# Optimization experiments

Measured on AMD Instinct MI355X. Metric: run time of the kernel, lower is better.

The kernel has to match this reference:

```python
import jax, jax.numpy as jnp
import numpy as np
import math

WINDOW = 2048
EMBED = 1024
BATCH = 8


def setup_inputs() -> dict:
    key = jax.random.key(0)
    ks = jax.random.split(key, 7)
    s = 1.0 / math.sqrt(EMBED)
    return {
        "embeddings": jax.random.normal(ks[0], (BATCH, WINDOW, EMBED), dtype=jnp.float32),
        "Wq": jax.random.uniform(ks[1], (EMBED, EMBED), jnp.float32, -s, s),
        "bq": jax.random.uniform(ks[2], (EMBED,), jnp.float32, -s, s),
        "Wk": jax.random.uniform(ks[3], (EMBED, EMBED), jnp.float32, -s, s),
        "bk": jax.random.uniform(ks[4], (EMBED,), jnp.float32, -s, s),
        "Wv": jax.random.uniform(ks[5], (EMBED, EMBED), jnp.float32, -s, s),
        "bv": jax.random.uniform(ks[6], (EMBED,), jnp.float32, -s, s),
    }


def reference(embeddings, Wq, bq, Wk, bk, Wv, bv):
    # Linear layers: x @ W.T + b (torch nn.Linear convention)
    Q = jnp.einsum('bse,fe->bsf', embeddings, Wq) + bq
    K = jnp.einsum('bse,fe->bsf', embeddings, Wk) + bk
    V = jnp.einsum('bse,fe->bsf', embeddings, Wv) + bv
    scale = 1.0 / math.sqrt(EMBED)
    # [B, S, S] score matrix: A[b, i, j] = Q_i . K_j / sqrt(d)
    A = jnp.einsum('bie,bje->bij', Q, K) * scale
    # causal additive mask: -inf where j > i (strictly upper triangular)
    mask = jnp.triu(jnp.full((WINDOW, WINDOW), -jnp.inf, dtype=A.dtype), k=1)
    A = A + mask
    # NOTE: faithful to original nn.Softmax(dim=1): normalize over QUERY axis
    P = jax.nn.softmax(A, axis=1)
    return jnp.einsum('bij,bje->bie', P, V)
```

## Files before the change

kernel.cpp:

```cpp
#include <hip/hip_runtime.h>
#include <stdint.h>

#define WINDOW 2048
#define EMBED  1024
#define BATCH  8
#define MTOT   (BATCH*WINDOW)

typedef unsigned short u16;
typedef __bf16 bf16x8 __attribute__((ext_vector_type(8)));
typedef float  f32x4  __attribute__((ext_vector_type(4)));

#define BM 256
#define BN 256
#define BK 64
#define HALF 8192
#define KSCALE 0.04508422717564447f

#define WAITVM4 asm volatile("s_waitcnt vmcnt(4)" ::: "memory")
#define WAITVM0 asm volatile("s_waitcnt vmcnt(0)" ::: "memory")

__device__ __forceinline__ u16 f2bf(float f) {
  union { float f; unsigned u; } a; a.f = f;
  unsigned r = a.u + 0x7FFF + ((a.u >> 16) & 1);
  return (u16)(r >> 16);
}
__device__ __forceinline__ float bf2f(u16 u) {
  union { unsigned u; float f; } a; a.u = ((unsigned)u) << 16;
  return a.f;
}

__device__ __forceinline__ void gload16(const u16* g, u16* l) {
  __builtin_amdgcn_global_load_lds(
      (const __attribute__((address_space(1))) unsigned int*)g,
      (__attribute__((address_space(3))) unsigned int*)l, 16, 0, 0);
}

__device__ __forceinline__ void stage_half(const u16* g, int ld, int kkc,
                                           u16* lb, int tid) {
  #pragma unroll
  for (int h = 0; h < 2; ++h) {
    int f = h * 512 + tid;
    int r = f >> 2, c = f & 3;
    gload16(g + (size_t)r * ld + kkc * 32 + ((c ^ ((r >> 1) & 3)) << 3),
            lb + f * 8);
  }
}

__device__ __forceinline__ void gemm256(
    const u16* __restrict__ A, int lda,
    const u16* __restrict__ B, int ldb,
    int nt, u16* lds, f32x4 acc[8][4])
{
  const int tid  = threadIdx.x;
  const int lane = tid & 63;
  const int wid  = tid >> 6;
  const int wm   = (wid >> 2) * 128;
  const int wn   = (wid & 3) * 64;
  const int lrow = lane & 15;
  const int hi   = lane >> 4;
  u16* LDA = lds;
  u16* LDB = lds + 4 * HALF;

  stage_half(A, lda, 0, LDA + 0 * HALF, tid);
  stage_half(B, ldb, 0, LDB + 0 * HALF, tid);
  stage_half(A, lda, 1, LDA + 1 * HALF, tid);
  stage_half(B, ldb, 1, LDB + 1 * HALF, tid);
  WAITVM4;
  __builtin_amdgcn_s_barrier();

  for (int t = 0; t < nt; ++t) {
    const int buf = (t & 1) * 2;
    const int nb  = ((t + 1) & 1) * 2;
    u16* LA0 = LDA + buf * HALF;
    u16* LA1 = LA0 + HALF;
    u16* LB0 = LDB + buf * HALF;
    u16* LB1 = LB0 + HALF;
    const bool s  = (t + 1) < nt;
    const u16* An = A + (size_t)(t + 1) * BK;
    const u16* Bn = B + (size_t)(t + 1) * BK;

    bf16x8 av[4], bv[4];

    #pragma unroll
    for (int mi = 0; mi < 4; ++mi) {
      int r = wm + mi * 16 + lrow;
      av[mi] = *(const bf16x8*)(LA0 + r * 32 + ((hi ^ ((r >> 1) & 3)) << 3));
    }
    #pragma unroll
    for (int ni = 0; ni < 4; ++ni) {
      int r = wn + ni * 16 + lrow;
      bv[ni] = *(const bf16x8*)(LB0 + r * 32 + ((hi ^ ((r >> 1) & 3)) << 3));
    }
    if (s) stage_half(An, lda, 0, LDA + nb * HALF, tid);
    __builtin_amdgcn_s_barrier();
    __builtin_amdgcn_s_setprio(1);
    #pragma unroll
    for (int mi = 0; mi < 4; ++mi)
      #pragma unroll
      for (int ni = 0; ni < 4; ++ni)
        acc[mi][ni] = __builtin_amdgcn_mfma_f32_16x16x32_bf16(av[mi], bv[ni], acc[mi][ni], 0, 0, 0);
    __builtin_amdgcn_s_setprio(0);
    __builtin_amdgcn_s_barrier();

    #pragma unroll
    for (int mi = 0; mi < 4; ++mi) {
      int r = wm + 64 + mi * 16 + lrow;
      av[mi] = *(const bf16x8*)(LA0 + r * 32 + ((hi ^ ((r >> 1) & 3)) << 3));
    }
    if (s) stage_half(Bn, ldb, 0, LDB + nb * HALF, tid);
    __builtin_amdgcn_s_barrier();
    __builtin_amdgcn_s_setprio(1);
    #pragma unroll
    for (int mi = 0; mi < 4; ++mi)
      #pragma unroll
      for (int ni = 0; ni < 4; ++ni)
        acc[4 + mi][ni] = __builtin_amdgcn_mfma_f32_16x16x32_bf16(av[mi], bv[ni], acc[4 + mi][ni], 0, 0, 0);
    __builtin_amdgcn_s_setprio(0);
    if (s) { WAITVM4; } else { WAITVM0; }
    __builtin_amdgcn_s_barrier();

    #pragma unroll
    for (int mi = 0; mi < 4; ++mi) {
      int r = wm + mi * 16 + lrow;
      av[mi] = *(const bf16x8*)(LA1 + r * 32 + ((hi ^ ((r >> 1) & 3)) << 3));
    }
    #pragma unroll
    for (int ni = 0; ni < 4; ++ni) {
      int r = wn + ni * 16 + lrow;
      bv[ni] = *(const bf16x8*)(LB1 + r * 32 + ((hi ^ ((r >> 1) & 3)) << 3));
    }
    if (s) stage_half(An, lda, 1, LDA + nb * HALF + HALF, tid);
    __builtin_amdgcn_s_barrier();
    __builtin_amdgcn_s_setprio(1);
    #pragma unroll
    for (int mi = 0; mi < 4; ++mi)
      #pragma unroll
      for (int ni = 0; ni < 4; ++ni)
        acc[mi][ni] = __builtin_amdgcn_mfma_f32_16x16x32_bf16(av[mi], bv[ni], acc[mi][ni], 0, 0, 0);
    __builtin_amdgcn_s_setprio(0);
    __builtin_amdgcn_s_barrier();

    #pragma unroll
    for (int mi = 0; mi < 4; ++mi) {
      int r = wm + 64 + mi * 16 + lrow;
      av[mi] = *(const bf16x8*)(LA1 + r * 32 + ((hi ^ ((r >> 1) & 3)) << 3));
    }
    if (s) stage_half(Bn, ldb, 1, LDB + nb * HALF + HALF, tid);
    __builtin_amdgcn_s_barrier();
    __builtin_amdgcn_s_setprio(1);
    #pragma unroll
    for (int mi = 0; mi < 4; ++mi)
      #pragma unroll
      for (int ni = 0; ni < 4; ++ni)
        acc[4 + mi][ni] = __builtin_amdgcn_mfma_f32_16x16x32_bf16(av[mi], bv[ni], acc[4 + mi][ni], 0, 0, 0);
    __builtin_amdgcn_s_setprio(0);
    if (s) { WAITVM4; }
    __builtin_amdgcn_s_barrier();
  }
}

__device__ __forceinline__ void zero_acc(f32x4 acc[8][4]) {
  const f32x4 z = {0.f, 0.f, 0.f, 0.f};
  #pragma unroll
  for (int i = 0; i < 8; ++i)
    #pragma unroll
    for (int j = 0; j < 4; ++j) acc[i][j] = z;
}

__global__ __launch_bounds__(256) void k_cvt(const float* __restrict__ in,
                                             u16* __restrict__ out, int n) {
  int i = (blockIdx.x * 256 + threadIdx.x) * 4;
  if (i >= n) return;
  float4 v = *(const float4*)(in + i);
  ushort4 o;
  o.x = f2bf(v.x); o.y = f2bf(v.y); o.z = f2bf(v.z); o.w = f2bf(v.w);
  *(ushort4*)(out + i) = o;
}

__global__ __launch_bounds__(512, 2) void k_qkv(
    const u16* __restrict__ Xb, const u16* __restrict__ Wb,
    const float* __restrict__ bq, const float* __restrict__ bk, const float* __restrict__ bv,
    u16* __restrict__ Q, u16* __restrict__ Ks, u16* __restrict__ V)
{
  __shared__ u16 lds[8 * HALF];
  const int m0 = blockIdx.x * BM;
  const int n0 = blockIdx.y * BN;
  const int z  = blockIdx.z;
  const u16*   W    = Wb + (size_t)z * EMBED * EMBED;
  const float* bias = (z == 0) ? bq : (z == 1) ? bk : bv;
  u16* out          = (z == 0) ? Q  : (z == 1) ? Ks : V;
  const float scale = (z == 1) ? KSCALE : 1.0f;

  f32x4 acc[8][4]; zero_acc(acc);
  gemm256(Xb + (size_t)m0 * EMBED, EMBED, W + (size_t)n0 * EMBED, EMBED,
          EMBED / BK, lds, acc);

  const int lane = threadIdx.x & 63, wid = threadIdx.x >> 6;
  const int wm = (wid >> 2) * 128, wn = (wid & 3) * 64;
  const int lrow = lane & 15, hi = lane >> 4;
  #pragma unroll
  for (int mi = 0; mi < 8; ++mi)
    #pragma unroll
    for (int ni = 0; ni < 4; ++ni)
      #pragma unroll
      for (int rr = 0; rr < 4; ++rr) {
        int gm = m0 + wm + mi * 16 + hi * 4 + rr;
        int gn = n0 + wn + ni * 16 + lrow;
        out[(size_t)gm * EMBED + gn] = f2bf((acc[mi][ni][rr] + bias[gn]) * scale);
      }
}

__global__ __launch_bounds__(512, 2) void k_spd(
    const u16* __restrict__ Q, const u16* __restrict__ Ks,
    u16* __restrict__ P, float* __restrict__ D)
{
  const int i0 = blockIdx.x * BM;
  const int j0 = blockIdx.y * BN;
  if (j0 > i0) return;
  const int b  = blockIdx.z;
  __shared__ u16 lds[8 * HALF];
  const u16* A = Q  + (size_t)b * WINDOW * EMBED + (size_t)i0 * EMBED;
  const u16* B = Ks + (size_t)b * WINDOW * EMBED + (size_t)j0 * EMBED;
  f32x4 acc[8][4]; zero_acc(acc);
  gemm256(A, EMBED, B, EMBED, EMBED / BK, lds, acc);

  u16* Pb   = P + (size_t)b * WINDOW * WINDOW;
  float* Db = D + (size_t)b * WINDOW;
  const int lane = threadIdx.x & 63, wid = threadIdx.x >> 6;
  const int wm = (wid >> 2) * 128, wn = (wid & 3) * 64;
  const int lrow = lane & 15, hi = lane >> 4;
  #pragma unroll
  for (int ni = 0; ni < 4; ++ni) {
    int gj = j0 + wn + ni * 16 + lrow;
    float csum = 0.f;
    #pragma unroll
    for (int mi = 0; mi < 8; ++mi)
      #pragma unroll
      for (int rr = 0; rr < 4; ++rr) {
        int gi = i0 + wm + mi * 16 + hi * 4 + rr;
        float p = (gi >= gj) ? exp2f(acc[mi][ni][rr]) : 0.0f;
        Pb[(size_t)gi * WINDOW + gj] = f2bf(p);
        csum += p;
      }
    csum += __shfl_xor(csum, 16, 64);
    csum += __shfl_xor(csum, 32, 64);
    if (hi == 0) atomicAdd(&Db[gj], csum);
  }
}

__global__ __launch_bounds__(256) void k_vdt(
    const u16* __restrict__ V, const float* __restrict__ D, u16* __restrict__ Vdt)
{
  __shared__ u16 tile[64][68];
  const int j0 = blockIdx.x * 64, e0 = blockIdx.y * 64, b = blockIdx.z;
  const u16* Vb = V   + (size_t)b * WINDOW * EMBED;
  u16* Tb       = Vdt + (size_t)b * EMBED * WINDOW;
  const float* Db = D + (size_t)b * WINDOW;
  const int t = threadIdx.x;
  const int rr = t >> 4;
  const int cc = (t & 15) * 4;
  #pragma unroll
  for (int p = 0; p < 4; ++p) {
    int r = p * 16 + rr;
    *(uint2*)&tile[r][cc] = *(const uint2*)(Vb + (size_t)(j0 + r) * EMBED + e0 + cc);
  }
  __syncthreads();
  #pragma unroll
  for (int p = 0; p < 4; ++p) {
    int er = p * 16 + rr;
    ushort4 o;
    o.x = f2bf(bf2f(tile[cc + 0][er]) / Db[j0 + cc + 0]);
    o.y = f2bf(bf2f(tile[cc + 1][er]) / Db[j0 + cc + 1]);
    o.z = f2bf(bf2f(tile[cc + 2][er]) / Db[j0 + cc + 2]);
    o.w = f2bf(bf2f(tile[cc + 3][er]) / Db[j0 + cc + 3]);
    *(ushort4*)(Tb + (size_t)(e0 + er) * WINDOW + j0 + cc) = o;
  }
}

__global__ __launch_bounds__(512, 2) void k_out(
    const u16* __restrict__ P, const u16* __restrict__ Vdt, float* __restrict__ O)
{
  __shared__ u16 lds[8 * HALF];
  const int i0 = ((int)gridDim.x - 1 - (int)blockIdx.x) * BM;
  const int e0 = blockIdx.y * BN;
  const int b  = blockIdx.z;
  const u16* A = P   + (size_t)b * WINDOW * WINDOW + (size_t)i0 * WINDOW;
  const u16* B = Vdt + (size_t)b * EMBED * WINDOW  + (size_t)e0 * WINDOW;
  f32x4 acc[8][4]; zero_acc(acc);
  gemm256(A, WINDOW, B, WINDOW, (i0 + BM) / BK, lds, acc);

  float* Ob = O + (size_t)b * WINDOW * EMBED;
  const int lane = threadIdx.x & 63, wid = threadIdx.x >> 6;
  const int wm = (wid >> 2) * 128, wn = (wid & 3) * 64;
  const int lrow = lane & 15, hi = lane >> 4;
  #pragma unroll
  for (int mi = 0; mi < 8; ++mi)
    #pragma unroll
    for (int ni = 0; ni < 4; ++ni)
      #pragma unroll
      for (int rr = 0; rr < 4; ++rr) {
        int gi = i0 + wm + mi * 16 + hi * 4 + rr;
        int ge = e0 + wn + ni * 16 + lrow;
        Ob[(size_t)gi * EMBED + ge] = acc[mi][ni][rr];
      }
}

extern "C" void kernel_launch(void* const* d_in, const int* in_sizes, int n_in,
                              void* d_out, int out_size, void* d_ws, size_t ws_size,
                              hipStream_t stream) {
  const float* X  = (const float*)d_in[0];
  const float* Wq = (const float*)d_in[1];
  const float* bq = (const float*)d_in[2];
  const float* Wk = (const float*)d_in[3];
  const float* bk = (const float*)d_in[4];
  const float* Wv = (const float*)d_in[5];
  const float* bv = (const float*)d_in[6];
  float* O = (float*)d_out;

  char* ws = (char*)d_ws;
  size_t off = 0;
  auto alloc = [&](size_t bytes) -> void* {
    void* p = ws + off; off += (bytes + 255) & ~(size_t)255; return p;
  };
  u16*  Xb  = (u16*)alloc((size_t)MTOT * EMBED * 2);
  u16*  Wb  = (u16*)alloc((size_t)3 * EMBED * EMBED * 2);
  u16*  Qb  = (u16*)alloc((size_t)MTOT * EMBED * 2);
  u16*  Kb  = (u16*)alloc((size_t)MTOT * EMBED * 2);
  u16*  Vb  = (u16*)alloc((size_t)MTOT * EMBED * 2);
  u16*  Vdt = (u16*)alloc((size_t)BATCH * EMBED * WINDOW * 2);
  u16*  P   = (u16*)alloc((size_t)BATCH * WINDOW * WINDOW * 2);
  float* D  = (float*)alloc((size_t)MTOT * 4);
  (void)ws_size; (void)in_sizes; (void)n_in; (void)out_size;

  k_cvt<<<dim3((MTOT * EMBED / 4 + 255) / 256), 256, 0, stream>>>(X, Xb, MTOT * EMBED);
  k_cvt<<<dim3((EMBED * EMBED / 4 + 255) / 256), 256, 0, stream>>>(Wq, Wb, EMBED * EMBED);
  k_cvt<<<dim3((EMBED * EMBED / 4 + 255) / 256), 256, 0, stream>>>(Wk, Wb + (size_t)EMBED * EMBED, EMBED * EMBED);
  k_cvt<<<dim3((EMBED * EMBED / 4 + 255) / 256), 256, 0, stream>>>(Wv, Wb + (size_t)2 * EMBED * EMBED, EMBED * EMBED);

  k_qkv<<<dim3(MTOT / BM, EMBED / BN, 3), 512, 0, stream>>>(Xb, Wb, bq, bk, bv, Qb, Kb, Vb);

  (void)hipMemsetAsync(D, 0, (size_t)MTOT * 4, stream);
  k_spd<<<dim3(WINDOW / BM, WINDOW / BN, BATCH), 512, 0, stream>>>(Qb, Kb, P, D);

  k_vdt<<<dim3(WINDOW / 64, EMBED / 64, BATCH), 256, 0, stream>>>(Vb, D, Vdt);

  k_out<<<dim3(WINDOW / BM, EMBED / BN, BATCH), 512, 0, stream>>>(P, Vdt, O);
}
```

Baseline: 303.6 us.

## Use 128x128 tiles for causal score and PV GEMMs, precompute load pointers

Adds a gemm128 path with 128x128 block tiles and 512 threads, used by the score/softmax-denominator and output GEMMs, with launch bounds raised to four blocks per CU. Smaller tiles make the causal triangle skipping finer-grained, so fewer masked elements are computed, and they give more blocks for load balancing. The global-to-LDS load addresses are now precomputed once and advanced per k-step instead of recomputed each stage. In exchange, each loaded element feeds fewer MFMAs per LDS byte, and each wave holds a smaller 64x32 accumulator tile.

```diff
diff --git a/kernel.cpp b/kernel.cpp
--- a/kernel.cpp
+++ b/kernel.cpp
@@ -10,14 +10,20 @@
 typedef __bf16 bf16x8 __attribute__((ext_vector_type(8)));
 typedef float  f32x4  __attribute__((ext_vector_type(4)));
 
-#define BM 256
-#define BN 256
 #define BK 64
-#define HALF 8192
 #define KSCALE 0.04508422717564447f
 
+#define BM2 256
+#define BN2 256
+#define HALF2 8192
+
+#define BM1 128
+#define HALF1 4096
+
 #define WAITVM4 asm volatile("s_waitcnt vmcnt(4)" ::: "memory")
+#define WAITVM2 asm volatile("s_waitcnt vmcnt(2)" ::: "memory")
 #define WAITVM0 asm volatile("s_waitcnt vmcnt(0)" ::: "memory")
+#define SBAR    __builtin_amdgcn_s_barrier()
 
 __device__ __forceinline__ u16 f2bf(float f) {
   union { float f; unsigned u; } a; a.f = f;
@@ -35,16 +41,6 @@
       (__attribute__((address_space(3))) unsigned int*)l, 16, 0, 0);
 }
 
-__device__ __forceinline__ void stage_half(const u16* g, int ld, int kkc,
-                                           u16* lb, int tid) {
-  #pragma unroll
-  for (int h = 0; h < 2; ++h) {
-    int f = h * 512 + tid;
-    int r = f >> 2, c = f & 3;
-    gload16(g + (size_t)r * ld + kkc * 32 + ((c ^ ((r >> 1) & 3)) << 3),
-            lb + f * 8);
-  }
-}
 
 __device__ __forceinline__ void gemm256(
     const u16* __restrict__ A, int lda,
@@ -58,27 +54,33 @@
   const int wn   = (wid & 3) * 64;
   const int lrow = lane & 15;
   const int hi   = lane >> 4;
-  u16* LDA = lds;
-  u16* LDB = lds + 4 * HALF;
-
-  stage_half(A, lda, 0, LDA + 0 * HALF, tid);
-  stage_half(B, ldb, 0, LDB + 0 * HALF, tid);
-  stage_half(A, lda, 1, LDA + 1 * HALF, tid);
-  stage_half(B, ldb, 1, LDB + 1 * HALF, tid);
+  u16* dA = lds;
+  u16* dB = lds + 4 * HALF2;
+
+  const int f0 = tid, f1 = 512 + tid;
+  const int r0 = f0 >> 2, r1 = f1 >> 2;
+  const int c0 = (((f0 & 3) ^ ((r0 >> 1) & 3)) << 3);
+  const int c1 = (((f1 & 3) ^ ((r1 >> 1) & 3)) << 3);
+  const u16* pA0 = A + (size_t)r0 * lda + c0;
+  const u16* pA1 = A + (size_t)r1 * lda + c1;
+  const u16* pB0 = B + (size_t)r0 * ldb + c0;
+  const u16* pB1 = B + (size_t)r1 * ldb + c1;
+  const int d0 = f0 * 8, d1 = f1 * 8;
+
+  gload16(pA0,      dA + d0); gload16(pA1,      dA + d1);
+  gload16(pB0,      dB + d0); gload16(pB1,      dB + d1);
+  gload16(pA0 + 32, dA + HALF2 + d0); gload16(pA1 + 32, dA + HALF2 + d1);
+  gload16(pB0 + 32, dB + HALF2 + d0); gload16(pB1 + 32, dB + HALF2 + d1);
+  pA0 += BK; pA1 += BK; pB0 += BK; pB1 += BK;
   WAITVM4;
-  __builtin_amdgcn_s_barrier();
+  SBAR;
 
   for (int t = 0; t < nt; ++t) {
-    const int buf = (t & 1) * 2;
-    const int nb  = ((t + 1) & 1) * 2;
-    u16* LA0 = LDA + buf * HALF;
-    u16* LA1 = LA0 + HALF;
-    u16* LB0 = LDB + buf * HALF;
-    u16* LB1 = LB0 + HALF;
-    const bool s  = (t + 1) < nt;
-    const u16* An = A + (size_t)(t + 1) * BK;
-    const u16* Bn = B + (size_t)(t + 1) * BK;
-
+    const int cur = (t & 1) * 2;
+    const int nxt = ((t + 1) & 1) * 2;
+    u16* LA0 = dA + cur * HALF2;  u16* LA1 = LA0 + HALF2;
+    u16* LB0 = dB + cur * HALF2;  u16* LB1 = LB0 + HALF2;
+    const bool s = (t + 1) < nt;
     bf16x8 av[4], bv[4];
 
     #pragma unroll
@@ -91,8 +93,8 @@
       int r = wn + ni * 16 + lrow;
       bv[ni] = *(const bf16x8*)(LB0 + r * 32 + ((hi ^ ((r >> 1) & 3)) << 3));
     }
-    if (s) stage_half(An, lda, 0, LDA + nb * HALF, tid);
-    __builtin_amdgcn_s_barrier();
+    if (s) { gload16(pA0, dA + nxt * HALF2 + d0); gload16(pA1, dA + nxt * HALF2 + d1); }
+    SBAR;
     __builtin_amdgcn_s_setprio(1);
     #pragma unroll
     for (int mi = 0; mi < 4; ++mi)
@@ -100,15 +102,15 @@
       for (int ni = 0; ni < 4; ++ni)
         acc[mi][ni] = __builtin_amdgcn_mfma_f32_16x16x32_bf16(av[mi], bv[ni], acc[mi][ni], 0, 0, 0);
     __builtin_amdgcn_s_setprio(0);
-    __builtin_amdgcn_s_barrier();
+    SBAR;
 
     #pragma unroll
     for (int mi = 0; mi < 4; ++mi) {
       int r = wm + 64 + mi * 16 + lrow;
       av[mi] = *(const bf16x8*)(LA0 + r * 32 + ((hi ^ ((r >> 1) & 3)) << 3));
     }
-    if (s) stage_half(Bn, ldb, 0, LDB + nb * HALF, tid);
-    __builtin_amdgcn_s_barrier();
+    if (s) { gload16(pB0, dB + nxt * HALF2 + d0); gload16(pB1, dB + nxt * HALF2 + d1); }
+    SBAR;
     __builtin_amdgcn_s_setprio(1);
     #pragma unroll
     for (int mi = 0; mi < 4; ++mi)
@@ -117,7 +119,7 @@
         acc[4 + mi][ni] = __builtin_amdgcn_mfma_f32_16x16x32_bf16(av[mi], bv[ni], acc[4 + mi][ni], 0, 0, 0);
     __builtin_amdgcn_s_setprio(0);
     if (s) { WAITVM4; } else { WAITVM0; }
-    __builtin_amdgcn_s_barrier();
+    SBAR;
 
     #pragma unroll
     for (int mi = 0; mi < 4; ++mi) {
@@ -129,8 +131,8 @@
       int r = wn + ni * 16 + lrow;
       bv[ni] = *(const bf16x8*)(LB1 + r * 32 + ((hi ^ ((r >> 1) & 3)) << 3));
     }
-    if (s) stage_half(An, lda, 1, LDA + nb * HALF + HALF, tid);
-    __builtin_amdgcn_s_barrier();
+    if (s) { gload16(pA0 + 32, dA + nxt * HALF2 + HALF2 + d0); gload16(pA1 + 32, dA + nxt * HALF2 + HALF2 + d1); }
+    SBAR;
     __builtin_amdgcn_s_setprio(1);
     #pragma unroll
     for (int mi = 0; mi < 4; ++mi)
@@ -138,15 +140,18 @@
       for (int ni = 0; ni < 4; ++ni)
         acc[mi][ni] = __builtin_amdgcn_mfma_f32_16x16x32_bf16(av[mi], bv[ni], acc[mi][ni], 0, 0, 0);
     __builtin_amdgcn_s_setprio(0);
-    __builtin_amdgcn_s_barrier();
+    SBAR;
 
     #pragma unroll
     for (int mi = 0; mi < 4; ++mi) {
       int r = wm + 64 + mi * 16 + lrow;
       av[mi] = *(const bf16x8*)(LA1 + r * 32 + ((hi ^ ((r >> 1) & 3)) << 3));
     }
-    if (s) stage_half(Bn, ldb, 1, LDB + nb * HALF + HALF, tid);
-    __builtin_amdgcn_s_barrier();
+    if (s) {
+      gload16(pB0 + 32, dB + nxt * HALF2 + HALF2 + d0); gload16(pB1 + 32, dB + nxt * HALF2 + HALF2 + d1);
+      pA0 += BK; pA1 += BK; pB0 += BK; pB1 += BK;
+    }
+    SBAR;
     __builtin_amdgcn_s_setprio(1);
     #pragma unroll
     for (int mi = 0; mi < 4; ++mi)
@@ -155,16 +160,93 @@
         acc[4 + mi][ni] = __builtin_amdgcn_mfma_f32_16x16x32_bf16(av[mi], bv[ni], acc[4 + mi][ni], 0, 0, 0);
     __builtin_amdgcn_s_setprio(0);
     if (s) { WAITVM4; }
-    __builtin_amdgcn_s_barrier();
+    SBAR;
   }
 }
 
-__device__ __forceinline__ void zero_acc(f32x4 acc[8][4]) {
-  const f32x4 z = {0.f, 0.f, 0.f, 0.f};
-  #pragma unroll
-  for (int i = 0; i < 8; ++i)
-    #pragma unroll
-    for (int j = 0; j < 4; ++j) acc[i][j] = z;
+__device__ __forceinline__ void gemm128(
+    const u16* __restrict__ A, int lda,
+    const u16* __restrict__ B, int ldb,
+    int nt, u16* lds, f32x4 acc[4][2])
+{
+  const int tid  = threadIdx.x;
+  const int lane = tid & 63;
+  const int wid  = tid >> 6;
+  const int wm   = (wid >> 2) * 64;
+  const int wn   = (wid & 3) * 32;
+  const int lrow = lane & 15;
+  const int hi   = lane >> 4;
+  u16* dA = lds;
+  u16* dB = lds + 4 * HALF1;
+
+  const int r = tid >> 2;
+  const int cs = (((tid & 3) ^ ((r >> 1) & 3)) << 3);
+  const u16* pA = A + (size_t)r * lda + cs;
+  const u16* pB = B + (size_t)r * ldb + cs;
+  const int d = tid * 8;
+
+  gload16(pA,      dA + d);         gload16(pB,      dB + d);
+  gload16(pA + 32, dA + HALF1 + d); gload16(pB + 32, dB + HALF1 + d);
+  pA += BK; pB += BK;
+  WAITVM2;
+  SBAR;
+
+  for (int t = 0; t < nt; ++t) {
+    const int cur = (t & 1) * 2;
+    const int nxt = ((t + 1) & 1) * 2;
+    u16* LA0 = dA + cur * HALF1;  u16* LA1 = LA0 + HALF1;
+    u16* LB0 = dB + cur * HALF1;  u16* LB1 = LB0 + HALF1;
+    const bool s = (t + 1) < nt;
+    bf16x8 av[4], bv[2];
+
+    #pragma unroll
+    for (int mi = 0; mi < 4; ++mi) {
+      int rr = wm + mi * 16 + lrow;
+      av[mi] = *(const bf16x8*)(LA0 + rr * 32 + ((hi ^ ((rr >> 1) & 3)) << 3));
+    }
+    #pragma unroll
+    for (int ni = 0; ni < 2; ++ni) {
+      int rr = wn + ni * 16 + lrow;
+      bv[ni] = *(const bf16x8*)(LB0 + rr * 32 + ((hi ^ ((rr >> 1) & 3)) << 3));
+    }
+    if (s) { gload16(pA, dA + nxt * HALF1 + d); gload16(pB, dB + nxt * HALF1 + d); }
+    SBAR;
+    __builtin_amdgcn_s_setprio(1);
+    #pragma unroll
+    for (int mi = 0; mi < 4; ++mi)
+      #pragma unroll
+      for (int ni = 0; ni < 2; ++ni)
+        acc[mi][ni] = __builtin_amdgcn_mfma_f32_16x16x32_bf16(av[mi], bv[ni], acc[mi][ni], 0, 0, 0);
+    __builtin_amdgcn_s_setprio(0);
+    if (s) { WAITVM2; } else { WAITVM0; }
+    SBAR;
+
+    #pragma unroll
+    for (int mi = 0; mi < 4; ++mi) {
+      int rr = wm + mi * 16 + lrow;
+      av[mi] = *(const bf16x8*)(LA1 + rr * 32 + ((hi ^ ((rr >> 1) & 3)) << 3));
+    }
+    #pragma unroll
+    for (int ni = 0; ni < 2; ++ni) {
+      int rr = wn + ni * 16 + lrow;
+      bv[ni] = *(const bf16x8*)(LB1 + rr * 32 + ((hi ^ ((rr >> 1) & 3)) << 3));
+    }
+    if (s) {
+      gload16(pA + 32, dA + nxt * HALF1 + HALF1 + d);
+      gload16(pB + 32, dB + nxt * HALF1 + HALF1 + d);
+      pA += BK; pB += BK;
+    }
+    SBAR;
+    __builtin_amdgcn_s_setprio(1);
+    #pragma unroll
+    for (int mi = 0; mi < 4; ++mi)
+      #pragma unroll
+      for (int ni = 0; ni < 2; ++ni)
+        acc[mi][ni] = __builtin_amdgcn_mfma_f32_16x16x32_bf16(av[mi], bv[ni], acc[mi][ni], 0, 0, 0);
+    __builtin_amdgcn_s_setprio(0);
+    if (s) { WAITVM2; }
+    SBAR;
+  }
 }
 
 __global__ __launch_bounds__(256) void k_cvt(const float* __restrict__ in,
@@ -182,16 +264,19 @@
     const float* __restrict__ bq, const float* __restrict__ bk, const float* __restrict__ bv,
     u16* __restrict__ Q, u16* __restrict__ Ks, u16* __restrict__ V)
 {
-  __shared__ u16 lds[8 * HALF];
-  const int m0 = blockIdx.x * BM;
-  const int n0 = blockIdx.y * BN;
+  __shared__ u16 lds[8 * HALF2];
+  const int m0 = blockIdx.x * BM2;
+  const int n0 = blockIdx.y * BN2;
   const int z  = blockIdx.z;
   const u16*   W    = Wb + (size_t)z * EMBED * EMBED;
   const float* bias = (z == 0) ? bq : (z == 1) ? bk : bv;
   u16* out          = (z == 0) ? Q  : (z == 1) ? Ks : V;
   const float scale = (z == 1) ? KSCALE : 1.0f;
 
-  f32x4 acc[8][4]; zero_acc(acc);
+  f32x4 acc[8][4];
+  const f32x4 zz = {0.f,0.f,0.f,0.f};
+  #pragma unroll
+  for (int i = 0; i < 8; ++i) for (int j = 0; j < 4; ++j) acc[i][j] = zz;
   gemm256(Xb + (size_t)m0 * EMBED, EMBED, W + (size_t)n0 * EMBED, EMBED,
           EMBED / BK, lds, acc);
 
@@ -210,31 +295,34 @@
       }
 }
 
-__global__ __launch_bounds__(512, 2) void k_spd(
+__global__ __launch_bounds__(512, 4) void k_spd(
     const u16* __restrict__ Q, const u16* __restrict__ Ks,
     u16* __restrict__ P, float* __restrict__ D)
 {
-  const int i0 = blockIdx.x * BM;
-  const int j0 = blockIdx.y * BN;
+  const int i0 = blockIdx.x * BM1;
+  const int j0 = blockIdx.y * BM1;
   if (j0 > i0) return;
   const int b  = blockIdx.z;
-  __shared__ u16 lds[8 * HALF];
+  __shared__ u16 lds[8 * HALF1];
   const u16* A = Q  + (size_t)b * WINDOW * EMBED + (size_t)i0 * EMBED;
   const u16* B = Ks + (size_t)b * WINDOW * EMBED + (size_t)j0 * EMBED;
-  f32x4 acc[8][4]; zero_acc(acc);
-  gemm256(A, EMBED, B, EMBED, EMBED / BK, lds, acc);
+  f32x4 acc[4][2];
+  const f32x4 zz = {0.f,0.f,0.f,0.f};
+  #pragma unroll
+  for (int i = 0; i < 4; ++i) for (int j = 0; j < 2; ++j) acc[i][j] = zz;
+  gemm128(A, EMBED, B, EMBED, EMBED / BK, lds, acc);
 
   u16* Pb   = P + (size_t)b * WINDOW * WINDOW;
   float* Db = D + (size_t)b * WINDOW;
   const int lane = threadIdx.x & 63, wid = threadIdx.x >> 6;
-  const int wm = (wid >> 2) * 128, wn = (wid & 3) * 64;
+  const int wm = (wid >> 2) * 64, wn = (wid & 3) * 32;
   const int lrow = lane & 15, hi = lane >> 4;
   #pragma unroll
-  for (int ni = 0; ni < 4; ++ni) {
+  for (int ni = 0; ni < 2; ++ni) {
     int gj = j0 + wn + ni * 16 + lrow;
     float csum = 0.f;
     #pragma unroll
-    for (int mi = 0; mi < 8; ++mi)
+    for (int mi = 0; mi < 4; ++mi)
       #pragma unroll
       for (int rr = 0; rr < 4; ++rr) {
         int gi = i0 + wm + mi * 16 + hi * 4 + rr;
@@ -277,26 +365,29 @@
   }
 }
 
-__global__ __launch_bounds__(512, 2) void k_out(
+__global__ __launch_bounds__(512, 4) void k_out(
     const u16* __restrict__ P, const u16* __restrict__ Vdt, float* __restrict__ O)
 {
-  __shared__ u16 lds[8 * HALF];
-  const int i0 = ((int)gridDim.x - 1 - (int)blockIdx.x) * BM;
-  const int e0 = blockIdx.y * BN;
+  __shared__ u16 lds[8 * HALF1];
+  const int i0 = ((int)gridDim.x - 1 - (int)blockIdx.x) * BM1;
+  const int e0 = blockIdx.y * BM1;
   const int b  = blockIdx.z;
   const u16* A = P   + (size_t)b * WINDOW * WINDOW + (size_t)i0 * WINDOW;
   const u16* B = Vdt + (size_t)b * EMBED * WINDOW  + (size_t)e0 * WINDOW;
-  f32x4 acc[8][4]; zero_acc(acc);
-  gemm256(A, WINDOW, B, WINDOW, (i0 + BM) / BK, lds, acc);
+  f32x4 acc[4][2];
+  const f32x4 zz = {0.f,0.f,0.f,0.f};
+  #pragma unroll
+  for (int i = 0; i < 4; ++i) for (int j = 0; j < 2; ++j) acc[i][j] = zz;
+  gemm128(A, WINDOW, B, WINDOW, (i0 + BM1) / BK, lds, acc);
 
   float* Ob = O + (size_t)b * WINDOW * EMBED;
   const int lane = threadIdx.x & 63, wid = threadIdx.x >> 6;
-  const int wm = (wid >> 2) * 128, wn = (wid & 3) * 64;
+  const int wm = (wid >> 2) * 64, wn = (wid & 3) * 32;
   const int lrow = lane & 15, hi = lane >> 4;
   #pragma unroll
-  for (int mi = 0; mi < 8; ++mi)
-    #pragma unroll
-    for (int ni = 0; ni < 4; ++ni)
+  for (int mi = 0; mi < 4; ++mi)
+    #pragma unroll
+    for (int ni = 0; ni < 2; ++ni)
       #pragma unroll
       for (int rr = 0; rr < 4; ++rr) {
         int gi = i0 + wm + mi * 16 + hi * 4 + rr;
@@ -337,12 +428,12 @@
   k_cvt<<<dim3((EMBED * EMBED / 4 + 255) / 256), 256, 0, stream>>>(Wk, Wb + (size_t)EMBED * EMBED, EMBED * EMBED);
   k_cvt<<<dim3((EMBED * EMBED / 4 + 255) / 256), 256, 0, stream>>>(Wv, Wb + (size_t)2 * EMBED * EMBED, EMBED * EMBED);
 
-  k_qkv<<<dim3(MTOT / BM, EMBED / BN, 3), 512, 0, stream>>>(Xb, Wb, bq, bk, bv, Qb, Kb, Vb);
+  k_qkv<<<dim3(MTOT / BM2, EMBED / BN2, 3), 512, 0, stream>>>(Xb, Wb, bq, bk, bv, Qb, Kb, Vb);
 
   (void)hipMemsetAsync(D, 0, (size_t)MTOT * 4, stream);
-  k_spd<<<dim3(WINDOW / BM, WINDOW / BN, BATCH), 512, 0, stream>>>(Qb, Kb, P, D);
+  k_spd<<<dim3(WINDOW / BM1, WINDOW / BM1, BATCH), 512, 0, stream>>>(Qb, Kb, P, D);
 
   k_vdt<<<dim3(WINDOW / 64, EMBED / 64, BATCH), 256, 0, stream>>>(Vb, D, Vdt);
 
-  k_out<<<dim3(WINDOW / BM, EMBED / BN, BATCH), 512, 0, stream>>>(P, Vdt, O);
-}
+  k_out<<<dim3(WINDOW / BM1, EMBED / BM1, BATCH), 512, 0, stream>>>(P, Vdt, O);
+}
```

Measured after the change: 314.7 us. 3.7% more time.
